# Optimization experiments

Measured on AMD Instinct MI355X. Metric: run time of the kernel, lower is better.

Reference implementation:

```python
import math
import jax, jax.numpy as jnp
import numpy as np

NUM_BUCKETS = 32
MAX_DISTANCE = 128
N_HEADS = 16
D_KV = 64


def relative_position_bucket(rel_pos, num_buckets=NUM_BUCKETS, max_distance=MAX_DISTANCE):
    # bidirectional=True path of the original
    n = -rel_pos
    nb = num_buckets // 2
    ret = (n < 0).astype(jnp.int32) * nb
    n = jnp.abs(n)
    max_exact = nb // 2
    is_small = n < max_exact
    val_large = max_exact + (
        jnp.log(n.astype(jnp.float32) / max_exact)
        / math.log(max_distance / max_exact)
        * (nb - max_exact)
    ).astype(jnp.int32)
    val_large = jnp.minimum(val_large, nb - 1)
    return jnp.where(is_small, n, val_large) + ret


def setup_inputs() -> dict:
    key = jax.random.key(0)
    ks = jax.random.split(key, 6)
    B, S, D = 2, 2048, 1024
    inner = N_HEADS * D_KV  # 1024
    sc = 1.0 / math.sqrt(D)
    return {
        "x": jax.random.normal(ks[0], (B, S, D), dtype=jnp.float32),
        "Wq": jax.random.normal(ks[1], (D, inner), dtype=jnp.float32) * sc,
        "Wk": jax.random.normal(ks[2], (D, inner), dtype=jnp.float32) * sc,
        "Wv": jax.random.normal(ks[3], (D, inner), dtype=jnp.float32) * sc,
        "Wo": jax.random.normal(ks[4], (inner, D), dtype=jnp.float32) * sc,
        "rel_table": jax.random.normal(ks[5], (NUM_BUCKETS, N_HEADS), dtype=jnp.float32),
        "attention_mask": jnp.zeros((B, 1, 1, S), dtype=jnp.float32),
    }


def reference(x, Wq, Wk, Wv, Wo, rel_table, attention_mask):
    B, S, D = x.shape
    H, Dk = N_HEADS, D_KV

    q = (x @ Wq).reshape(B, S, H, Dk).transpose(0, 2, 1, 3)  # bhqd
    k = (x @ Wk).reshape(B, S, H, Dk).transpose(0, 2, 1, 3)
    v = (x @ Wv).reshape(B, S, H, Dk).transpose(0, 2, 1, 3)

    # NOTE: T5 attention has no 1/sqrt(d) scaling
    scores = jnp.einsum('bhqd,bhkd->bhqk', q.astype(jnp.float32), k.astype(jnp.float32))

    pos = jnp.arange(S)
    rel_pos = pos[None, :] - pos[:, None]  # [S,S] = k_pos - q_pos
    buckets = relative_position_bucket(rel_pos)
    position_bias = jnp.transpose(rel_table[buckets], (2, 0, 1))  # [H,S,S]

    scores = scores + position_bias[None, ...] + attention_mask
    weights = jax.nn.softmax(scores, axis=-1)
    out = jnp.einsum('bhqk,bhkd->bhqd', weights, v.astype(jnp.float32))
    out = out.transpose(0, 2, 1, 3).reshape(B, S, H * Dk).astype(x.dtype)
    out = out @ Wo
    return (out, position_bias)
```

## Files before the change

kernel.cpp:

```cpp
#include <hip/hip_runtime.h>
#include <hip/hip_bf16.h>
#include <math.h>
#include <stdint.h>

typedef __bf16 bf16_t;
typedef __attribute__((ext_vector_type(8))) __bf16 bf16x8;
typedef __attribute__((ext_vector_type(4))) float f32x4;
typedef unsigned short u16;
typedef unsigned int u32;

#define DEV static __device__ __forceinline__
#define LOG2E 1.4426950408889634f

DEV u16 f2b(float f){ bf16_t h = (bf16_t)f; return __builtin_bit_cast(u16, h); }
DEV float b2f(u16 u){ bf16_t h = __builtin_bit_cast(bf16_t, u); return (float)h; }
DEV f32x4 mfma16(bf16x8 a, bf16x8 b, f32x4 c){
  return __builtin_amdgcn_mfma_f32_16x16x32_bf16(a, b, c, 0, 0, 0);
}

#if __has_builtin(__builtin_amdgcn_exp2f)
DEV float fexp2(float x){ return __builtin_amdgcn_exp2f(x); }
#else
DEV float fexp2(float x){ return exp2f(x); }
#endif

DEV void gld16(const void* g, void* l){
  __builtin_amdgcn_global_load_lds((const __attribute__((address_space(1))) u32*)g,
                                   (__attribute__((address_space(3))) u32*)l, 16, 0, 0);
}

DEV bf16x8 ldsA64(const u16* arr, int row, int ch){
  return *(const bf16x8*)&arr[row*64 + ((ch ^ (row&7))*8)];
}
DEV bf16x8 ldsA32(const u16* arr, int row, int ch){
  return *(const bf16x8*)&arr[row*32 + ((ch ^ ((row>>1)&3))*8)];
}

__global__ __launch_bounds__(256) void k_prep(const float* __restrict__ x,
                                              const float* __restrict__ Wq, const float* __restrict__ Wk,
                                              const float* __restrict__ Wv, const float* __restrict__ Wo,
                                              const float* __restrict__ rel_table, const float* __restrict__ mask,
                                              u16* __restrict__ xh, u16* __restrict__ xl,
                                              u16* __restrict__ wth, u16* __restrict__ wot,
                                              float* __restrict__ bt, float* __restrict__ bt2,
                                              float* __restrict__ msk2){
  __shared__ float tile[64][65];
  int bid = blockIdx.x;
  int t = threadIdx.x;
  if(bid < 4096){
    size_t i = ((size_t)bid*256 + t)*4;
    float4 v = *(const float4*)(x + i);
    ushort4 hv, lv; float f, hf;
    f=v.x; hv.x=f2b(f); hf=b2f(hv.x); lv.x=f2b(f-hf);
    f=v.y; hv.y=f2b(f); hf=b2f(hv.y); lv.y=f2b(f-hf);
    f=v.z; hv.z=f2b(f); hf=b2f(hv.z); lv.z=f2b(f-hf);
    f=v.w; hv.w=f2b(f); hf=b2f(hv.w); lv.w=f2b(f-hf);
    *(ushort4*)(xh+i) = hv;
    *(ushort4*)(xl+i) = lv;
  } else if(bid < 5120){
    int rr = bid - 4096;
    int z = rr >> 8, ky = (rr >> 4) & 15, nx = rr & 15;
    const float* W = (z==0)?Wq:((z==1)?Wk:((z==2)?Wv:Wo));
    int n0 = nx*64, k0 = ky*64;
    int r = t>>6, c = t&63;
    #pragma unroll
    for(int i=0;i<16;i++){
      int row = i*4 + r;
      tile[row][c] = W[(size_t)(k0+row)*1024 + n0 + c];
    }
    __syncthreads();
    #pragma unroll
    for(int i=0;i<16;i++){
      int nrow = i*4 + r;
      float v = tile[c][nrow];
      size_t o = (size_t)(n0+nrow)*1024 + k0 + c;
      if(z<3) wth[(size_t)z*1048576 + o] = f2b(v);
      else    wot[o] = f2b(v);
    }
  } else {
    int gid = (bid-5120)*256 + t;
    if(gid < 4096) msk2[gid] = mask[gid]*LOG2E;
    int h = gid >> 12, idx = gid & 4095;
    float v = 0.f;
    if(idx < 4095){
      int delta = idx - 2047;
      int n = -delta;
      int ret = 0;
      if(n < 0){ ret = 16; n = -n; }
      int bucket;
      if(n < 8) bucket = n + ret;
      else {
        float a = (float)log((double)n * 0.125);
        float rr2 = (float)((double)a / (double)2.7725887298583984f);
        int vl = 8 + (int)(rr2 * 8.0f);
        vl = vl > 15 ? 15 : vl;
        bucket = vl + ret;
      }
      v = rel_table[bucket*16 + h];
    }
    bt[gid] = v;
    bt2[gid] = v*LOG2E - 32.0f;
  }
}

__global__ __launch_bounds__(256) void k_write_bias(const float* __restrict__ bt,
                                                    float* __restrict__ out){
  size_t f = ((size_t)blockIdx.x*256 + threadIdx.x)*4;
  int h = (int)(f >> 22);
  int rem = (int)(f & 4194303);
  int q = rem >> 11;
  int k = rem & 2047;
  const float* row = bt + h*4096 + (k - q + 2047);
  float4 v = make_float4(row[0], row[1], row[2], row[3]);
  *(float4*)(out + f) = v;
}

__global__ __launch_bounds__(256) void k_gemm_qkv(const u16* __restrict__ xh, const u16* __restrict__ xl,
                                                  const u16* __restrict__ wth,
                                                  u16* __restrict__ qh, u16* __restrict__ ql,
                                                  u16* __restrict__ kh, u16* __restrict__ vt){
  __shared__ __align__(16) u16 SM[17408];
  u16* Ah = SM; u16* Al = SM+4096; u16* Bh = SM+8192;
  int z = blockIdx.z;
  const u16* WH = wth + (size_t)z*1048576;
  int m0 = blockIdx.y*128, n0 = blockIdx.x*128;
  int t = threadIdx.x, w = t>>6, lane = t&63, l16 = lane&15, g = lane>>4;
  f32x4 acc[4][4];
  #pragma unroll
  for(int i=0;i<4;i++)
    #pragma unroll
    for(int j=0;j<4;j++) acc[i][j] = {0.f,0.f,0.f,0.f};
  int rbase = (w>>1)*64, cbase = (w&1)*64;
  for(int k0=0;k0<1024;k0+=32){
    __syncthreads();
    #pragma unroll
    for(int jj=0;jj<6;jj++){
      int q = w + 4*jj;
      int arr = q>>3, sub = q&7;
      if(z!=0 && arr==1) continue;
      int row = sub*16 + (lane>>2);
      int lch = (lane&3) ^ ((row>>1)&3);
      const u16* src;
      if(arr==0)      src = xh + (size_t)(m0+row)*1024 + k0 + lch*8;
      else if(arr==1) src = xl + (size_t)(m0+row)*1024 + k0 + lch*8;
      else            src = WH + (size_t)(n0+row)*1024 + k0 + lch*8;
      gld16(src, &SM[q*512]);
    }
    __syncthreads();
    if(z!=0){
      bf16x8 ah[4];
      #pragma unroll
      for(int i=0;i<4;i++) ah[i] = ldsA32(Ah, rbase + i*16 + l16, g);
      #pragma unroll
      for(int j=0;j<4;j++){
        bf16x8 bh = ldsA32(Bh, cbase + j*16 + l16, g);
        #pragma unroll
        for(int i=0;i<4;i++)
          acc[i][j] = mfma16(ah[i], bh, acc[i][j]);
      }
    } else {
      bf16x8 ah[4], am[4];
      #pragma unroll
      for(int i=0;i<4;i++){
        int row = rbase + i*16 + l16;
        ah[i] = ldsA32(Ah, row, g);
        am[i] = ldsA32(Al, row, g);
      }
      #pragma unroll
      for(int j=0;j<4;j++){
        bf16x8 bh = ldsA32(Bh, cbase + j*16 + l16, g);
        #pragma unroll
        for(int i=0;i<4;i++){
          acc[i][j] = mfma16(ah[i], bh, acc[i][j]);
          acc[i][j] = mfma16(am[i], bh, acc[i][j]);
        }
      }
    }
  }
  if(z==2){
    __syncthreads();
    #pragma unroll
    for(int i=0;i<4;i++)
      #pragma unroll
      for(int j=0;j<4;j++)
        #pragma unroll
        for(int r=0;r<4;r++){
          int ml = rbase + i*16 + g*4 + r;
          int nl = cbase + j*16 + l16;
          SM[nl*136 + ml] = f2b(acc[i][j][r]);
        }
    __syncthreads();
    int bb = m0 >> 11;
    #pragma unroll
    for(int kk=0;kk<8;kk++){
      int id = t + 256*kk;
      int row = id>>4, ch = id&15;
      uint4 v = *(const uint4*)&SM[row*136 + ch*8];
      int n = n0 + row;
      size_t dst = ((size_t)(bb*16 + (n>>6))*64 + (n&63))*2048 + (m0&2047) + ch*8;
      *(uint4*)&vt[dst] = v;
    }
  } else {
    #pragma unroll
    for(int i=0;i<4;i++)
      #pragma unroll
      for(int j=0;j<4;j++)
        #pragma unroll
        for(int r=0;r<4;r++){
          int m = m0 + rbase + i*16 + g*4 + r;
          int n = n0 + cbase + j*16 + l16;
          float v = acc[i][j][r];
          if(z==0) v *= LOG2E;
          int b = m >> 11, s = m & 2047;
          int hh = n >> 6, d = n & 63;
          size_t a = ((size_t)(b*16+hh)*2048 + s)*64 + d;
          u16 hb = f2b(v);
          if(z==0){ qh[a]=hb; ql[a]=f2b(v - b2f(hb)); }
          else    { kh[a]=hb; }
        }
  }
}

__global__ __launch_bounds__(256) void k_attn(const u16* __restrict__ qh, const u16* __restrict__ ql,
                                              const u16* __restrict__ kh,
                                              const u16* __restrict__ vt, const float* __restrict__ bt2,
                                              const float* __restrict__ msk2,
                                              float* __restrict__ Op, float* __restrict__ rsp){
  __shared__ __align__(16) u16 SM[17408];
  u16* KH = SM; u16* VT = SM+4096;
  int bh = blockIdx.y, b = bh>>4, h = bh&15;
  int q0 = blockIdx.x*128;
  int kha = blockIdx.z;
  int t = threadIdx.x, w = t>>6, lane = t&63, l16 = lane&15, g = lane>>4;
  size_t base  = (size_t)bh*2048*64;
  size_t vbase = (size_t)bh*64*2048;
  u16* PSw = SM + 8192 + w*2304;
  const float* bt2h = bt2 + h*4096;
  const float* msk2b = msk2 + b*2048;

  bf16x8 qfh[2][2], qfl[2][2];
  #pragma unroll
  for(int i=0;i<2;i++){
    int qr = q0 + w*32 + i*16 + l16;
    size_t a0 = base + (size_t)qr*64 + g*8;
    qfh[i][0] = *(const bf16x8*)&qh[a0];
    qfl[i][0] = *(const bf16x8*)&ql[a0];
    qfh[i][1] = *(const bf16x8*)&qh[a0+32];
    qfl[i][1] = *(const bf16x8*)&ql[a0+32];
  }
  f32x4 O[2][4];
  float rs[2][4];
  #pragma unroll
  for(int i=0;i<2;i++){
    #pragma unroll
    for(int jd=0;jd<4;jd++) O[i][jd] = {0.f,0.f,0.f,0.f};
    #pragma unroll
    for(int r=0;r<4;r++) rs[i][r] = 0.f;
  }

  int kend = kha*1024 + 1024;
  for(int k0=kha*1024; k0<kend; k0+=64){
    __syncthreads();
    #pragma unroll
    for(int jj=0;jj<4;jj++){
      int q = w + 4*jj;
      int arr = q>>3, sub = q&7;
      int row = sub*8 + (lane>>3);
      int lch = (lane&7) ^ (row&7);
      const u16* src;
      if(arr==0) src = kh + base + (size_t)(k0+row)*64 + lch*8;
      else       src = vt + vbase + (size_t)row*2048 + k0 + lch*8;
      gld16(src, &SM[q*512]);
    }
    float mkj[4];
    #pragma unroll
    for(int j=0;j<4;j++) mkj[j] = msk2b[k0 + j*16 + l16];
    f32x4 sc[2][4];
    #pragma unroll
    for(int i=0;i<2;i++){
      const float* bb = bt2h + (k0 + l16 + 2047 - (q0 + w*32 + i*16 + g*4));
      #pragma unroll
      for(int j=0;j<4;j++){
        #pragma unroll
        for(int r=0;r<4;r++)
          sc[i][j][r] = bb[j*16 - r] + mkj[j];
      }
    }
    __syncthreads();
    #pragma unroll
    for(int j=0;j<4;j++){
      int krow = j*16 + l16;
      bf16x8 kfh0 = ldsA64(KH, krow, g);
      bf16x8 kfh1 = ldsA64(KH, krow, 4+g);
      #pragma unroll
      for(int i=0;i<2;i++){
        f32x4 s = sc[i][j];
        s = mfma16(qfh[i][0], kfh0, s);
        s = mfma16(qfl[i][0], kfh0, s);
        s = mfma16(qfh[i][1], kfh1, s);
        s = mfma16(qfl[i][1], kfh1, s);
        sc[i][j] = s;
      }
    }
    #pragma unroll
    for(int i=0;i<2;i++){
      #pragma unroll
      for(int j=0;j<4;j++){
        #pragma unroll
        for(int r=0;r<4;r++){
          float p = fexp2(sc[i][j][r]);
          rs[i][r] += p;
          PSw[(i*16 + g*4 + r)*72 + j*16 + l16] = f2b(p);
        }
      }
    }
    #pragma unroll
    for(int ds=0; ds<2; ds++){
      bf16x8 pa0 = *(const bf16x8*)&PSw[(     l16)*72 + ds*32 + g*8];
      bf16x8 pa1 = *(const bf16x8*)&PSw[(16 + l16)*72 + ds*32 + g*8];
      #pragma unroll
      for(int jd=0;jd<4;jd++){
        bf16x8 vb = ldsA64(VT, jd*16 + l16, ds*4 + g);
        O[0][jd] = mfma16(pa0, vb, O[0][jd]);
        O[1][jd] = mfma16(pa1, vb, O[1][jd]);
      }
    }
  }
  size_t pbase = ((size_t)kha*32 + bh)*2048;
  #pragma unroll
  for(int i=0;i<2;i++){
    #pragma unroll
    for(int r=0;r<4;r++){
      float v = rs[i][r];
      v += __shfl_xor(v,1,64);
      v += __shfl_xor(v,2,64);
      v += __shfl_xor(v,4,64);
      v += __shfl_xor(v,8,64);
      int q = q0 + w*32 + i*16 + g*4 + r;
      size_t oo = (pbase + q)*64;
      #pragma unroll
      for(int jd=0;jd<4;jd++)
        Op[oo + jd*16 + l16] = O[i][jd][r];
      if(l16==0) rsp[pbase + q] = v;
    }
  }
}

__global__ __launch_bounds__(256) void k_combine(const float* __restrict__ Op, const float* __restrict__ rsp,
                                                 u16* __restrict__ ao){
  size_t fid = ((size_t)blockIdx.x*256 + threadIdx.x)*4;
  int m = (int)(fid >> 10), n = (int)(fid & 1023);
  int bh = (m>>11)*16 + (n>>6);
  int q = m & 2047, d = n & 63;
  size_t po = ((size_t)bh*2048 + q)*64 + d;
  f32x4 a = *(const f32x4*)&Op[po];
  f32x4 c = *(const f32x4*)&Op[po + 4194304];
  float inv = 1.f/(rsp[bh*2048 + q] + rsp[bh*2048 + q + 65536]);
  ushort4 o;
  o.x = f2b((a[0]+c[0])*inv);
  o.y = f2b((a[1]+c[1])*inv);
  o.z = f2b((a[2]+c[2])*inv);
  o.w = f2b((a[3]+c[3])*inv);
  *(ushort4*)&ao[fid] = o;
}

__global__ __launch_bounds__(256) void k_gemm_out(const u16* __restrict__ ao, const u16* __restrict__ wot,
                                                  float* __restrict__ out){
  __shared__ __align__(16) u16 SM[8192];
  u16* As = SM; u16* Bs = SM+4096;
  int m0 = blockIdx.y*128, n0 = blockIdx.x*128;
  int t = threadIdx.x, w = t>>6, lane = t&63, l16 = lane&15, g = lane>>4;
  f32x4 acc[4][4];
  #pragma unroll
  for(int i=0;i<4;i++)
    #pragma unroll
    for(int j=0;j<4;j++) acc[i][j] = {0.f,0.f,0.f,0.f};
  int rbase = (w>>1)*64, cbase = (w&1)*64;
  for(int k0=0;k0<1024;k0+=32){
    __syncthreads();
    #pragma unroll
    for(int jj=0;jj<4;jj++){
      int q = w + 4*jj;
      int arr = q>>3, sub = q&7;
      int row = sub*16 + (lane>>2);
      int lch = (lane&3) ^ ((row>>1)&3);
      const u16* src;
      if(arr==0) src = ao  + (size_t)(m0+row)*1024 + k0 + lch*8;
      else       src = wot + (size_t)(n0+row)*1024 + k0 + lch*8;
      gld16(src, &SM[q*512]);
    }
    __syncthreads();
    bf16x8 af[4];
    #pragma unroll
    for(int i=0;i<4;i++) af[i] = ldsA32(As, rbase + i*16 + l16, g);
    #pragma unroll
    for(int j=0;j<4;j++){
      bf16x8 bfb = ldsA32(Bs, cbase + j*16 + l16, g);
      #pragma unroll
      for(int i=0;i<4;i++)
        acc[i][j] = mfma16(af[i], bfb, acc[i][j]);
    }
  }
  #pragma unroll
  for(int i=0;i<4;i++)
    #pragma unroll
    for(int j=0;j<4;j++)
      #pragma unroll
      for(int r=0;r<4;r++){
        int m = m0 + rbase + i*16 + g*4 + r;
        int n = n0 + cbase + j*16 + l16;
        out[(size_t)m*1024 + n] = acc[i][j][r];
      }
}

extern "C" void kernel_launch(void* const* d_in, const int* in_sizes, int n_in,
                              void* d_out, int out_size, void* d_ws, size_t ws_size,
                              hipStream_t stream) {
  const float* x   = (const float*)d_in[0];
  const float* Wq  = (const float*)d_in[1];
  const float* Wk  = (const float*)d_in[2];
  const float* Wv  = (const float*)d_in[3];
  const float* Wo  = (const float*)d_in[4];
  const float* rel = (const float*)d_in[5];
  const float* msk = (const float*)d_in[6];
  float* out = (float*)d_out;
  float* bias_out = out + (size_t)4194304;
  char* ws = (char*)d_ws;
  u16* xh  = (u16*)(ws + 0);
  u16* xl  = (u16*)(ws + 8388608);
  u16* wth = (u16*)(ws + 16777216);
  u16* wot = (u16*)(ws + 23068672);
  u16* qh  = (u16*)(ws + 25165824);
  u16* ql  = (u16*)(ws + 33554432);
  u16* kh  = (u16*)(ws + 41943040);
  u16* vt  = (u16*)(ws + 50331648);
  u16* ao  = (u16*)(ws + 58720256);
  float* Op  = (float*)(ws + 67108864);
  float* rsp = (float*)(ws + 100663296);
  float* bt  = (float*)(ws + 101187584);
  float* bt2 = (float*)(ws + 101449728);
  float* msk2= (float*)(ws + 101711872);

  k_prep      <<<5376, 256, 0, stream>>>(x, Wq, Wk, Wv, Wo, rel, msk,
                                         xh, xl, wth, wot, bt, bt2, msk2);
  k_write_bias<<<65536, 256, 0, stream>>>(bt, bias_out);
  k_gemm_qkv  <<<dim3(8,32,3), 256, 0, stream>>>(xh, xl, wth, qh, ql, kh, vt);
  k_attn      <<<dim3(16,32,2), 256, 0, stream>>>(qh, ql, kh, vt, bt2, msk2, Op, rsp);
  k_combine   <<<4096, 256, 0, stream>>>(Op, rsp, ao);
  k_gemm_out  <<<dim3(8,32), 256, 0, stream>>>(ao, wot, out);
}
```

Baseline: 516.3 us.

## Replace split-K attention with full-K smaller query tiles and fused normalization

The attention kernel no longer splits the key range across two blocks. Each block now handles 64 queries (16 per wave) over all 2048 keys and normalizes its output directly into the bf16 buffer, which removes the k_combine kernel and the fp32 partial-output round trip through global memory. The bias is now read with one vectorized 4-float load. The block count stays the same and per-wave register use drops, but each K/V tile loaded into shared memory now serves half as many queries, so global-to-LDS traffic per FLOP doubles.

```diff
diff --git a/kernel.cpp b/kernel.cpp
--- a/kernel.cpp
+++ b/kernel.cpp
@@ -6,6 +6,7 @@
 typedef __bf16 bf16_t;
 typedef __attribute__((ext_vector_type(8))) __bf16 bf16x8;
 typedef __attribute__((ext_vector_type(4))) float f32x4;
+typedef float f32x4a __attribute__((ext_vector_type(4), aligned(4)));
 typedef unsigned short u16;
 typedef unsigned int u32;
 
@@ -225,41 +226,36 @@
                                               const u16* __restrict__ kh,
                                               const u16* __restrict__ vt, const float* __restrict__ bt2,
                                               const float* __restrict__ msk2,
-                                              float* __restrict__ Op, float* __restrict__ rsp){
-  __shared__ __align__(16) u16 SM[17408];
+                                              u16* __restrict__ ao){
+  __shared__ __align__(16) u16 SM[12800];
   u16* KH = SM; u16* VT = SM+4096;
   int bh = blockIdx.y, b = bh>>4, h = bh&15;
-  int q0 = blockIdx.x*128;
-  int kha = blockIdx.z;
+  int q0 = blockIdx.x*64;
   int t = threadIdx.x, w = t>>6, lane = t&63, l16 = lane&15, g = lane>>4;
   size_t base  = (size_t)bh*2048*64;
   size_t vbase = (size_t)bh*64*2048;
-  u16* PSw = SM + 8192 + w*2304;
+  u16* PSw = SM + 8192 + w*1152;
   const float* bt2h = bt2 + h*4096;
   const float* msk2b = msk2 + b*2048;
 
-  bf16x8 qfh[2][2], qfl[2][2];
-  #pragma unroll
-  for(int i=0;i<2;i++){
-    int qr = q0 + w*32 + i*16 + l16;
+  bf16x8 qfh[2], qfl[2];
+  {
+    int qr = q0 + w*16 + l16;
     size_t a0 = base + (size_t)qr*64 + g*8;
-    qfh[i][0] = *(const bf16x8*)&qh[a0];
-    qfl[i][0] = *(const bf16x8*)&ql[a0];
-    qfh[i][1] = *(const bf16x8*)&qh[a0+32];
-    qfl[i][1] = *(const bf16x8*)&ql[a0+32];
-  }
-  f32x4 O[2][4];
-  float rs[2][4];
-  #pragma unroll
-  for(int i=0;i<2;i++){
-    #pragma unroll
-    for(int jd=0;jd<4;jd++) O[i][jd] = {0.f,0.f,0.f,0.f};
-    #pragma unroll
-    for(int r=0;r<4;r++) rs[i][r] = 0.f;
-  }
-
-  int kend = kha*1024 + 1024;
-  for(int k0=kha*1024; k0<kend; k0+=64){
+    qfh[0] = *(const bf16x8*)&qh[a0];
+    qfl[0] = *(const bf16x8*)&ql[a0];
+    qfh[1] = *(const bf16x8*)&qh[a0+32];
+    qfl[1] = *(const bf16x8*)&ql[a0+32];
+  }
+  f32x4 O[4];
+  float rs[4];
+  #pragma unroll
+  for(int jd=0;jd<4;jd++) O[jd] = {0.f,0.f,0.f,0.f};
+  #pragma unroll
+  for(int r=0;r<4;r++) rs[r] = 0.f;
+  int qgbase = q0 + w*16 + g*4;
+
+  for(int k0=0;k0<2048;k0+=64){
     __syncthreads();
     #pragma unroll
     for(int jj=0;jj<4;jj++){
@@ -272,18 +268,14 @@
       else       src = vt + vbase + (size_t)row*2048 + k0 + lch*8;
       gld16(src, &SM[q*512]);
     }
-    float mkj[4];
-    #pragma unroll
-    for(int j=0;j<4;j++) mkj[j] = msk2b[k0 + j*16 + l16];
-    f32x4 sc[2][4];
-    #pragma unroll
-    for(int i=0;i<2;i++){
-      const float* bb = bt2h + (k0 + l16 + 2047 - (q0 + w*32 + i*16 + g*4));
+    f32x4 sc[4];
+    {
+      const float* bb = bt2h + (k0 + l16 + 2047 - qgbase);
       #pragma unroll
       for(int j=0;j<4;j++){
-        #pragma unroll
-        for(int r=0;r<4;r++)
-          sc[i][j][r] = bb[j*16 - r] + mkj[j];
+        f32x4a ld = *(const f32x4a*)(bb + j*16 - 3);
+        float mk = msk2b[k0 + j*16 + l16];
+        sc[j] = (f32x4){ld[3]+mk, ld[2]+mk, ld[1]+mk, ld[0]+mk};
       }
     }
     __syncthreads();
@@ -292,76 +284,46 @@
       int krow = j*16 + l16;
       bf16x8 kfh0 = ldsA64(KH, krow, g);
       bf16x8 kfh1 = ldsA64(KH, krow, 4+g);
-      #pragma unroll
-      for(int i=0;i<2;i++){
-        f32x4 s = sc[i][j];
-        s = mfma16(qfh[i][0], kfh0, s);
-        s = mfma16(qfl[i][0], kfh0, s);
-        s = mfma16(qfh[i][1], kfh1, s);
-        s = mfma16(qfl[i][1], kfh1, s);
-        sc[i][j] = s;
-      }
-    }
-    #pragma unroll
-    for(int i=0;i<2;i++){
-      #pragma unroll
-      for(int j=0;j<4;j++){
-        #pragma unroll
-        for(int r=0;r<4;r++){
-          float p = fexp2(sc[i][j][r]);
-          rs[i][r] += p;
-          PSw[(i*16 + g*4 + r)*72 + j*16 + l16] = f2b(p);
-        }
+      f32x4 s = sc[j];
+      s = mfma16(qfh[0], kfh0, s);
+      s = mfma16(qfl[0], kfh0, s);
+      s = mfma16(qfh[1], kfh1, s);
+      s = mfma16(qfl[1], kfh1, s);
+      sc[j] = s;
+    }
+    #pragma unroll
+    for(int j=0;j<4;j++){
+      #pragma unroll
+      for(int r=0;r<4;r++){
+        float p = fexp2(sc[j][r]);
+        rs[r] += p;
+        PSw[(g*4+r)*72 + j*16 + l16] = f2b(p);
       }
     }
     #pragma unroll
     for(int ds=0; ds<2; ds++){
-      bf16x8 pa0 = *(const bf16x8*)&PSw[(     l16)*72 + ds*32 + g*8];
-      bf16x8 pa1 = *(const bf16x8*)&PSw[(16 + l16)*72 + ds*32 + g*8];
+      bf16x8 pa = *(const bf16x8*)&PSw[l16*72 + ds*32 + g*8];
       #pragma unroll
       for(int jd=0;jd<4;jd++){
         bf16x8 vb = ldsA64(VT, jd*16 + l16, ds*4 + g);
-        O[0][jd] = mfma16(pa0, vb, O[0][jd]);
-        O[1][jd] = mfma16(pa1, vb, O[1][jd]);
-      }
-    }
-  }
-  size_t pbase = ((size_t)kha*32 + bh)*2048;
-  #pragma unroll
-  for(int i=0;i<2;i++){
-    #pragma unroll
-    for(int r=0;r<4;r++){
-      float v = rs[i][r];
-      v += __shfl_xor(v,1,64);
-      v += __shfl_xor(v,2,64);
-      v += __shfl_xor(v,4,64);
-      v += __shfl_xor(v,8,64);
-      int q = q0 + w*32 + i*16 + g*4 + r;
-      size_t oo = (pbase + q)*64;
-      #pragma unroll
-      for(int jd=0;jd<4;jd++)
-        Op[oo + jd*16 + l16] = O[i][jd][r];
-      if(l16==0) rsp[pbase + q] = v;
-    }
-  }
-}
-
-__global__ __launch_bounds__(256) void k_combine(const float* __restrict__ Op, const float* __restrict__ rsp,
-                                                 u16* __restrict__ ao){
-  size_t fid = ((size_t)blockIdx.x*256 + threadIdx.x)*4;
-  int m = (int)(fid >> 10), n = (int)(fid & 1023);
-  int bh = (m>>11)*16 + (n>>6);
-  int q = m & 2047, d = n & 63;
-  size_t po = ((size_t)bh*2048 + q)*64 + d;
-  f32x4 a = *(const f32x4*)&Op[po];
-  f32x4 c = *(const f32x4*)&Op[po + 4194304];
-  float inv = 1.f/(rsp[bh*2048 + q] + rsp[bh*2048 + q + 65536]);
-  ushort4 o;
-  o.x = f2b((a[0]+c[0])*inv);
-  o.y = f2b((a[1]+c[1])*inv);
-  o.z = f2b((a[2]+c[2])*inv);
-  o.w = f2b((a[3]+c[3])*inv);
-  *(ushort4*)&ao[fid] = o;
+        O[jd] = mfma16(pa, vb, O[jd]);
+      }
+    }
+  }
+  #pragma unroll
+  for(int r=0;r<4;r++){
+    float v = rs[r];
+    v += __shfl_xor(v,1,64);
+    v += __shfl_xor(v,2,64);
+    v += __shfl_xor(v,4,64);
+    v += __shfl_xor(v,8,64);
+    float inv = 1.f/v;
+    int q = qgbase + r;
+    size_t a = ((size_t)(b*2048 + q))*1024 + h*64;
+    #pragma unroll
+    for(int jd=0;jd<4;jd++)
+      ao[a + jd*16 + l16] = f2b(O[jd][r]*inv);
+  }
 }
 
 __global__ __launch_bounds__(256) void k_gemm_out(const u16* __restrict__ ao, const u16* __restrict__ wot,
@@ -435,17 +397,14 @@
   u16* kh  = (u16*)(ws + 41943040);
   u16* vt  = (u16*)(ws + 50331648);
   u16* ao  = (u16*)(ws + 58720256);
-  float* Op  = (float*)(ws + 67108864);
-  float* rsp = (float*)(ws + 100663296);
-  float* bt  = (float*)(ws + 101187584);
-  float* bt2 = (float*)(ws + 101449728);
-  float* msk2= (float*)(ws + 101711872);
+  float* bt  = (float*)(ws + 67108864);
+  float* bt2 = (float*)(ws + 67371008);
+  float* msk2= (float*)(ws + 67633152);
 
   k_prep      <<<5376, 256, 0, stream>>>(x, Wq, Wk, Wv, Wo, rel, msk,
                                          xh, xl, wth, wot, bt, bt2, msk2);
   k_write_bias<<<65536, 256, 0, stream>>>(bt, bias_out);
   k_gemm_qkv  <<<dim3(8,32,3), 256, 0, stream>>>(xh, xl, wth, qh, ql, kh, vt);
-  k_attn      <<<dim3(16,32,2), 256, 0, stream>>>(qh, ql, kh, vt, bt2, msk2, Op, rsp);
-  k_combine   <<<4096, 256, 0, stream>>>(Op, rsp, ao);
+  k_attn      <<<dim3(32,32), 256, 0, stream>>>(qh, ql, kh, vt, bt2, msk2, ao);
   k_gemm_out  <<<dim3(8,32), 256, 0, stream>>>(ao, wot, out);
 }
```

Result: no change. 509.0 us (-1.4%).
